# Kernel optimization log

Measured on AMD Instinct MI355X. Metric: run time of the kernel, lower is better.

## Reference

```python
import jax, jax.numpy as jnp
import numpy as np

N_PATIENT = 50000
N_GENE = 20000
N_EDGE = 640000
P_DIM, G_DIM, H, OUT = 64, 32, 128, 8


def setup_inputs() -> dict:
    key = jax.random.key(0)
    ks = jax.random.split(key, 20)
    s = 0.02
    return {
        "x_patient": jax.random.normal(ks[0], (N_PATIENT, P_DIM), jnp.float32),
        "x_gene": jax.random.normal(ks[1], (N_GENE, G_DIM), jnp.float32),
        "edge_index": jax.random.randint(ks[2], (2, N_EDGE), 0, N_GENE, jnp.int32),
        # patient MLP
        "W_p1": jax.random.normal(ks[3], (P_DIM, H), jnp.float32) * s,
        "b_p1": jnp.zeros((H,), jnp.float32),
        "W_p2": jax.random.normal(ks[4], (H, H), jnp.float32) * s,
        "b_p2": jnp.zeros((H,), jnp.float32),
        # gene MLP
        "W_g1": jax.random.normal(ks[5], (G_DIM, H), jnp.float32) * s,
        "b_g1": jnp.zeros((H,), jnp.float32),
        "W_g2": jax.random.normal(ks[6], (H, H), jnp.float32) * s,
        "b_g2": jnp.zeros((H,), jnp.float32),
        # SAGEConv 1: lin_l acts on aggregated src, lin_r (root) on dst
        "W1_l": jax.random.normal(ks[7], (H, H), jnp.float32) * s,
        "b1_l": jnp.zeros((H,), jnp.float32),
        "W1_r": jax.random.normal(ks[8], (H, H), jnp.float32) * s,
        # SAGEConv 2
        "W2_l": jax.random.normal(ks[9], (H, H), jnp.float32) * s,
        "b2_l": jnp.zeros((H,), jnp.float32),
        "W2_r": jax.random.normal(ks[10], (H, H), jnp.float32) * s,
        # final fc
        "W_fc": jax.random.normal(ks[11], (H, OUT), jnp.float32) * s,
        "b_fc": jnp.zeros((OUT,), jnp.float32),
    }


def reference(x_patient, x_gene, edge_index,
              W_p1, b_p1, W_p2, b_p2,
              W_g1, b_g1, W_g2, b_g2,
              W1_l, b1_l, W1_r,
              W2_l, b2_l, W2_r,
              W_fc, b_fc):
    # node-type MLPs
    p = jax.nn.relu(x_patient @ W_p1 + b_p1) @ W_p2 + b_p2   # [N_P, H]
    g = jax.nn.relu(x_gene @ W_g1 + b_g1) @ W_g2 + b_g2       # [N_G, H]

    src, dst = edge_index[0], edge_index[1]
    # gene_x is unchanged between layers, so the sum-aggregate is identical
    # for both SAGEConv layers: compute the gather + segment-sum once.
    agg = jax.ops.segment_sum(g[src], dst, num_segments=x_patient.shape[0])  # [N_P, H]

    # SAGEConv(aggr='sum'): out = lin_l(agg) + lin_r(x_dst), bias in lin_l
    p = jax.nn.relu(agg @ W1_l + b1_l + p @ W1_r)
    p = jax.nn.relu(agg @ W2_l + b2_l + p @ W2_r)
    return p @ W_fc + b_fc  # [N_P, OUT]
```

## Files before the change

### kernel.cpp

```cpp
#include <hip/hip_runtime.h>

#define NP 50000
#define NG 20000
#define NE 640000
#define PD 64
#define GD 32
#define HD 128
#define OD 8
#define CAP 96
#define FILLB 125
#define EPB 5120
#define GENE_TILES 313
#define ROW0_NOAGG 20096
#define AGGPAD (ROW0_NOAGG - NG)
#define PATALLB 782

using f32x4 = __attribute__((ext_vector_type(4))) float;
using s16x8 = __attribute__((ext_vector_type(8))) short;

__device__ __forceinline__ unsigned short f2bf(float f) {
    union { float f; unsigned u; } v; v.f = f;
    const unsigned r = v.u + 0x7FFFu + ((v.u >> 16) & 1u);
    return (unsigned short)(r >> 16);
}
__device__ __forceinline__ float bfpair_lo(unsigned v) {
    union { unsigned u; float f; } x; x.u = v << 16; return x.f;
}
__device__ __forceinline__ float bfpair_hi(unsigned v) {
    union { unsigned u; float f; } x; x.u = v & 0xFFFF0000u; return x.f;
}

#define TOT_SWZ 112640

__global__ __launch_bounds__(256) void swz_kernel(
    const float* __restrict__ Wp1, const float* __restrict__ Wp2,
    const float* __restrict__ W1l, const float* __restrict__ W1r,
    const float* __restrict__ W2l, const float* __restrict__ W2r,
    const float* __restrict__ Wfc,
    const float* __restrict__ Wg1, const float* __restrict__ Wg2,
    unsigned short* __restrict__ wswz, unsigned short* __restrict__ aggb)
{
    const int u = blockIdx.x * 256 + threadIdx.x;
    if (u < TOT_SWZ) {
        const float* src; int K, Nr, doff;
        if      (u <   8192) { src = Wp1; K =  64; Nr = HD; doff = 0; }
        else if (u <  24576) { src = Wp2; K = 128; Nr = HD; doff = 8192; }
        else if (u <  40960) { src = W1l; K = 128; Nr = HD; doff = 24576; }
        else if (u <  57344) { src = W1r; K = 128; Nr = HD; doff = 40960; }
        else if (u <  73728) { src = W2l; K = 128; Nr = HD; doff = 57344; }
        else if (u <  90112) { src = W2r; K = 128; Nr = HD; doff = 73728; }
        else if (u <  92160) { src = Wfc; K = 128; Nr = OD; doff = 90112; }
        else if (u <  96256) { src = Wg1; K =  32; Nr = HD; doff = 92160; }
        else                 { src = Wg2; K = 128; Nr = HD; doff = 96256; }
        const int e  = u - doff;
        const int j  = e & 7;
        const int ln = (e >> 3) & 63;
        const int f  = e >> 9;
        const int KC = K >> 5;
        const int c  = f % KC;
        const int n0 = f / KC;
        const int k  = c * 32 + (ln >> 4) * 8 + j;
        const int n  = n0 * 16 + (ln & 15);
        wswz[u] = f2bf((n < Nr) ? src[k * Nr + n] : 0.f);
    } else {
        aggb[(size_t)NG * HD + (u - TOT_SWZ)] = 0;
    }
}

__global__ __launch_bounds__(256) void genefill_kernel(
    const float* __restrict__ xg,
    const unsigned short* __restrict__ wswz,
    const float* __restrict__ bg1, const float* __restrict__ bg2,
    unsigned short* __restrict__ g,
    const int* __restrict__ ei, unsigned short* __restrict__ hist16)
{
    __shared__ __align__(16) char smem[20480];
    const int tid = threadIdx.x;
    if (blockIdx.x >= GENE_TILES) {
        int* cnt = (int*)smem;
#pragma unroll
        for (int k = 0; k < 5; ++k) {
            const int idx = k * 256 + tid;
            if (idx < NG / 16) ((int4*)cnt)[idx] = (int4){0, 0, 0, 0};
        }
        __syncthreads();
        const int fb = blockIdx.x - GENE_TILES;
        const int base = fb * EPB;
#pragma unroll
        for (int it = 0; it < 5; ++it) {
            const int e0 = base + it * 1024 + tid;
            const int d0 = ei[NE + e0];
            const int d1 = ei[NE + e0 + 256];
            const int d2 = ei[NE + e0 + 512];
            const int d3 = ei[NE + e0 + 768];
            atomicAdd(&cnt[d0 >> 2], 1 << ((d0 & 3) * 8));
            atomicAdd(&cnt[d1 >> 2], 1 << ((d1 & 3) * 8));
            atomicAdd(&cnt[d2 >> 2], 1 << ((d2 & 3) * 8));
            atomicAdd(&cnt[d3 >> 2], 1 << ((d3 & 3) * 8));
        }
        __syncthreads();
        unsigned short* Hb = hist16 + fb * NG;
#pragma unroll
        for (int k = 0; k < 20; ++k) {
            const int idx = k * 256 + tid;
            if (idx < NG / 4) {
                const unsigned w = (unsigned)cnt[idx];
                int2 o;
                o.x = (int)((w & 0xFFu) | ((w & 0xFF00u) << 8));
                o.y = (int)(((w >> 16) & 0xFFu) | (((w >> 24) & 0xFFu) << 16));
                ((int2*)Hb)[idx] = o;
            }
        }
        return;
    }
    const unsigned short* wg1 = wswz + 92160;
    const unsigned short* wg2 = wswz + 96256;

    const int lane = tid & 63;
    const int wid  = tid >> 6;
    const int quad = lane >> 4;
    const int l16  = lane & 15;
    const int row0 = blockIdx.x * 64 + wid * 16;
    const int arow = min(row0 + l16, NG - 1);
    unsigned short* X = (unsigned short*)smem + wid * 16 * 136;
    const f32x4 Z = {0.f, 0.f, 0.f, 0.f};

    s16x8 a;
    {
        const float* xr = xg + (size_t)arow * GD + quad * 8;
        const f32x4 u0 = *(const f32x4*)xr;
        const f32x4 u1 = *(const f32x4*)(xr + 4);
#pragma unroll
        for (int j = 0; j < 4; ++j) {
            a[j]     = (short)f2bf(u0[j]);
            a[4 + j] = (short)f2bf(u1[j]);
        }
    }
    f32x4 C[8];
#pragma unroll
    for (int n = 0; n < 8; ++n) {
        const s16x8 b = *(const s16x8*)&wg1[(n * 64 + lane) * 8];
        C[n] = __builtin_amdgcn_mfma_f32_16x16x32_bf16(a, b, Z, 0, 0, 0);
    }
#pragma unroll
    for (int n = 0; n < 8; ++n) {
        const float bias = bg1[n * 16 + l16];
#pragma unroll
        for (int r = 0; r < 4; ++r)
            X[(quad * 4 + r) * 136 + n * 16 + l16] = f2bf(fmaxf(C[n][r] + bias, 0.f));
    }
    __syncthreads();
    s16x8 pa[4];
#pragma unroll
    for (int c = 0; c < 4; ++c) pa[c] = *(const s16x8*)&X[l16 * 136 + c * 32 + quad * 8];
#pragma unroll
    for (int n = 0; n < 8; ++n) {
        C[n] = Z;
#pragma unroll
        for (int c = 0; c < 4; ++c) {
            const s16x8 b = *(const s16x8*)&wg2[((n * 4 + c) * 64 + lane) * 8];
            C[n] = __builtin_amdgcn_mfma_f32_16x16x32_bf16(pa[c], b, C[n], 0, 0, 0);
        }
    }
#pragma unroll
    for (int n = 0; n < 8; ++n) {
        const float bias = bg2[n * 16 + l16];
#pragma unroll
        for (int r = 0; r < 4; ++r) {
            const int row = row0 + quad * 4 + r;
            if (row < NG) g[(size_t)row * HD + n * 16 + l16] = f2bf(C[n][r] + bias);
        }
    }
}

__global__ __launch_bounds__(256) void scan_kernel(
    unsigned short* __restrict__ hist16, int* __restrict__ cursor)
{
    const int d = blockIdx.x * 256 + threadIdx.x;
    if (d >= NG) return;
    int run = 0;
#pragma unroll 5
    for (int b = 0; b < FILLB; ++b) {
        const int t = hist16[b * NG + d];
        hist16[b * NG + d] = (unsigned short)run;
        run += t;
    }
    cursor[d] = run;
}

__global__ __launch_bounds__(256) void place_kernel(
    const int* __restrict__ ei, const unsigned short* __restrict__ hist16,
    unsigned short* __restrict__ pad)
{
    __shared__ __align__(16) int cnt[NG / 2];
    const int tid = threadIdx.x;
    const int* Hb = (const int*)(hist16 + blockIdx.x * NG);
#pragma unroll
    for (int k = 0; k < 10; ++k) {
        const int idx = k * 256 + tid;
        if (idx < NG / 8) ((int4*)cnt)[idx] = ((const int4*)Hb)[idx];
    }
    __syncthreads();
    const int base = blockIdx.x * EPB;
#pragma unroll
    for (int it = 0; it < 5; ++it) {
        const int e0 = base + it * 1024 + tid;
        const int s0 = ei[e0];       const int d0 = ei[NE + e0];
        const int s1 = ei[e0 + 256]; const int d1 = ei[NE + e0 + 256];
        const int s2 = ei[e0 + 512]; const int d2 = ei[NE + e0 + 512];
        const int s3 = ei[e0 + 768]; const int d3 = ei[NE + e0 + 768];
        { const int o = atomicAdd(&cnt[d0 >> 1], 1 << ((d0 & 1) * 16));
          const int p = (o >> ((d0 & 1) * 16)) & 0xFFFF;
          if (p < CAP) pad[d0 * CAP + p] = (unsigned short)s0; }
        { const int o = atomicAdd(&cnt[d1 >> 1], 1 << ((d1 & 1) * 16));
          const int p = (o >> ((d1 & 1) * 16)) & 0xFFFF;
          if (p < CAP) pad[d1 * CAP + p] = (unsigned short)s1; }
        { const int o = atomicAdd(&cnt[d2 >> 1], 1 << ((d2 & 1) * 16));
          const int p = (o >> ((d2 & 1) * 16)) & 0xFFFF;
          if (p < CAP) pad[d2 * CAP + p] = (unsigned short)s2; }
        { const int o = atomicAdd(&cnt[d3 >> 1], 1 << ((d3 & 1) * 16));
          const int p = (o >> ((d3 & 1) * 16)) & 0xFFFF;
          if (p < CAP) pad[d3 * CAP + p] = (unsigned short)s3; }
    }
}

__global__ __launch_bounds__(256) void agg_kernel(
    const int* __restrict__ cursor, const unsigned short* __restrict__ pad,
    const unsigned short* __restrict__ g, unsigned short* __restrict__ aggb)
{
    const int row  = blockIdx.x * 4 + (threadIdx.x >> 6);
    const int lane = threadIdx.x & 63;
    const int grp  = lane >> 4;
    const int sub  = lane & 15;

    float acc[8] = {0.f, 0.f, 0.f, 0.f, 0.f, 0.f, 0.f, 0.f};
    const int cnt = min(cursor[row], CAP);
    const size_t rb = (size_t)row * CAP;
    for (int i = grp * 4; i < cnt; i += 16) {
        const ushort4 q = *(const ushort4*)&pad[rb + i];
        int r0 = q.x, r1 = q.y, r2 = q.z, r3 = q.w;
        const bool v1 = (i + 1) < cnt, v2 = (i + 2) < cnt, v3 = (i + 3) < cnt;
        r1 = v1 ? r1 : r0;  r2 = v2 ? r2 : r0;  r3 = v3 ? r3 : r0;
        const float s1 = v1 ? 1.f : 0.f, s2 = v2 ? 1.f : 0.f, s3 = v3 ? 1.f : 0.f;
        const s16x8 g0 = *(const s16x8*)&g[(size_t)r0 * HD + sub * 8];
        const s16x8 g1 = *(const s16x8*)&g[(size_t)r1 * HD + sub * 8];
        const s16x8 g2 = *(const s16x8*)&g[(size_t)r2 * HD + sub * 8];
        const s16x8 g3 = *(const s16x8*)&g[(size_t)r3 * HD + sub * 8];
        const unsigned* d0 = (const unsigned*)&g0;
        const unsigned* d1 = (const unsigned*)&g1;
        const unsigned* d2 = (const unsigned*)&g2;
        const unsigned* d3 = (const unsigned*)&g3;
#pragma unroll
        for (int k = 0; k < 4; ++k) {
            acc[2 * k]     += bfpair_lo(d0[k]);
            acc[2 * k + 1] += bfpair_hi(d0[k]);
            acc[2 * k]     = fmaf(bfpair_lo(d1[k]), s1, acc[2 * k]);
            acc[2 * k + 1] = fmaf(bfpair_hi(d1[k]), s1, acc[2 * k + 1]);
            acc[2 * k]     = fmaf(bfpair_lo(d2[k]), s2, acc[2 * k]);
            acc[2 * k + 1] = fmaf(bfpair_hi(d2[k]), s2, acc[2 * k + 1]);
            acc[2 * k]     = fmaf(bfpair_lo(d3[k]), s3, acc[2 * k]);
            acc[2 * k + 1] = fmaf(bfpair_hi(d3[k]), s3, acc[2 * k + 1]);
        }
    }
#pragma unroll
    for (int k = 0; k < 8; ++k) {
        acc[k] += __shfl_xor(acc[k], 16);
        acc[k] += __shfl_xor(acc[k], 32);
    }
    if (lane < 16) {
        unsigned o[4];
#pragma unroll
        for (int k = 0; k < 4; ++k)
            o[k] = (unsigned)f2bf(acc[2 * k]) | ((unsigned)f2bf(acc[2 * k + 1]) << 16);
        *(int4*)&aggb[(size_t)row * HD + lane * 8] = *(int4*)o;
    }
}

__global__ __launch_bounds__(256) void patall_kernel(
    const float* __restrict__ xp, const unsigned short* __restrict__ aggb,
    const unsigned short* __restrict__ wswz,
    const float* __restrict__ bp1, const float* __restrict__ bp2,
    const float* __restrict__ b1l, const float* __restrict__ b2l,
    const float* __restrict__ bfc,
    float* __restrict__ out)
{
    const unsigned short* wp1 = wswz + 0;
    const unsigned short* wp2 = wswz + 8192;
    const unsigned short* w1l = wswz + 24576;
    const unsigned short* w1r = wswz + 40960;
    const unsigned short* w2l = wswz + 57344;
    const unsigned short* w2r = wswz + 73728;
    const unsigned short* wfc = wswz + 90112;

    __shared__ __align__(16) unsigned short XA[64 * 136];

    const int tid  = threadIdx.x;
    const int lane = tid & 63;
    const int wid  = tid >> 6;
    const int quad = lane >> 4;
    const int l16  = lane & 15;
    const int brow = blockIdx.x * 64;
    const bool hasAgg = (brow < NG);
    const int nA = wid * 2, nB = wid * 2 + 1;
    const f32x4 Z = {0.f, 0.f, 0.f, 0.f};

#pragma unroll
    for (int s = 0; s < 4; ++s) {
        const int slot = s * 256 + tid;
        const int r  = slot >> 4;
        const int cv = slot & 15;
        const f32x4 u = *(const f32x4*)&xp[(size_t)min(brow + r, NP - 1) * PD + cv * 4];
        unsigned short o[4];
#pragma unroll
        for (int j = 0; j < 4; ++j) o[j] = f2bf(u[j]);
        *(ushort4*)&XA[r * 136 + cv * 4] = *(ushort4*)o;
    }
    __syncthreads();

    f32x4 acc[4][2];

#pragma unroll
    for (int rt = 0; rt < 4; ++rt) { acc[rt][0] = Z; acc[rt][1] = Z; }
#pragma unroll
    for (int c = 0; c < 2; ++c) {
        const s16x8 b0 = *(const s16x8*)&wp1[((nA * 2 + c) * 64 + lane) * 8];
        const s16x8 b1 = *(const s16x8*)&wp1[((nB * 2 + c) * 64 + lane) * 8];
#pragma unroll
        for (int rt = 0; rt < 4; ++rt) {
            const s16x8 a = *(const s16x8*)&XA[(rt * 16 + l16) * 136 + c * 32 + quad * 8];
            acc[rt][0] = __builtin_amdgcn_mfma_f32_16x16x32_bf16(a, b0, acc[rt][0], 0, 0, 0);
            acc[rt][1] = __builtin_amdgcn_mfma_f32_16x16x32_bf16(a, b1, acc[rt][1], 0, 0, 0);
        }
    }
    __syncthreads();
#pragma unroll
    for (int t = 0; t < 2; ++t) {
        const int n = wid * 2 + t;
        const float bias = bp1[n * 16 + l16];
#pragma unroll
        for (int rt = 0; rt < 4; ++rt)
#pragma unroll
            for (int r = 0; r < 4; ++r)
                XA[(rt * 16 + quad * 4 + r) * 136 + n * 16 + l16] =
                    f2bf(fmaxf(acc[rt][t][r] + bias, 0.f));
    }
    __syncthreads();

#pragma unroll
    for (int rt = 0; rt < 4; ++rt) { acc[rt][0] = Z; acc[rt][1] = Z; }
#pragma unroll
    for (int c = 0; c < 4; ++c) {
        const s16x8 b0 = *(const s16x8*)&wp2[((nA * 4 + c) * 64 + lane) * 8];
        const s16x8 b1 = *(const s16x8*)&wp2[((nB * 4 + c) * 64 + lane) * 8];
#pragma unroll
        for (int rt = 0; rt < 4; ++rt) {
            const s16x8 a = *(const s16x8*)&XA[(rt * 16 + l16) * 136 + c * 32 + quad * 8];
            acc[rt][0] = __builtin_amdgcn_mfma_f32_16x16x32_bf16(a, b0, acc[rt][0], 0, 0, 0);
            acc[rt][1] = __builtin_amdgcn_mfma_f32_16x16x32_bf16(a, b1, acc[rt][1], 0, 0, 0);
        }
    }
    __syncthreads();
#pragma unroll
    for (int t = 0; t < 2; ++t) {
        const int n = wid * 2 + t;
        const float bias = bp2[n * 16 + l16];
#pragma unroll
        for (int rt = 0; rt < 4; ++rt)
#pragma unroll
            for (int r = 0; r < 4; ++r)
                XA[(rt * 16 + quad * 4 + r) * 136 + n * 16 + l16] =
                    f2bf(acc[rt][t][r] + bias);
    }
    __syncthreads();

    if (hasAgg) {
#pragma unroll
        for (int rt = 0; rt < 4; ++rt) { acc[rt][0] = Z; acc[rt][1] = Z; }
#pragma unroll
        for (int c = 0; c < 4; ++c) {
            const s16x8 br0 = *(const s16x8*)&w1r[((nA * 4 + c) * 64 + lane) * 8];
            const s16x8 br1 = *(const s16x8*)&w1r[((nB * 4 + c) * 64 + lane) * 8];
            const s16x8 bl0 = *(const s16x8*)&w1l[((nA * 4 + c) * 64 + lane) * 8];
            const s16x8 bl1 = *(const s16x8*)&w1l[((nB * 4 + c) * 64 + lane) * 8];
#pragma unroll
            for (int rt = 0; rt < 4; ++rt) {
                const s16x8 ap = *(const s16x8*)&XA[(rt * 16 + l16) * 136 + c * 32 + quad * 8];
                const s16x8 ag = *(const s16x8*)&aggb[(size_t)(brow + rt * 16 + l16) * HD + c * 32 + quad * 8];
                acc[rt][0] = __builtin_amdgcn_mfma_f32_16x16x32_bf16(ap, br0, acc[rt][0], 0, 0, 0);
                acc[rt][0] = __builtin_amdgcn_mfma_f32_16x16x32_bf16(ag, bl0, acc[rt][0], 0, 0, 0);
                acc[rt][1] = __builtin_amdgcn_mfma_f32_16x16x32_bf16(ap, br1, acc[rt][1], 0, 0, 0);
                acc[rt][1] = __builtin_amdgcn_mfma_f32_16x16x32_bf16(ag, bl1, acc[rt][1], 0, 0, 0);
            }
        }
        __syncthreads();
#pragma unroll
        for (int t = 0; t < 2; ++t) {
            const int n = wid * 2 + t;
            const float bias = b1l[n * 16 + l16];
#pragma unroll
            for (int rt = 0; rt < 4; ++rt)
#pragma unroll
                for (int r = 0; r < 4; ++r)
                    XA[(rt * 16 + quad * 4 + r) * 136 + n * 16 + l16] =
                        f2bf(fmaxf(acc[rt][t][r] + bias, 0.f));
        }
        __syncthreads();

#pragma unroll
        for (int rt = 0; rt < 4; ++rt) { acc[rt][0] = Z; acc[rt][1] = Z; }
#pragma unroll
        for (int c = 0; c < 4; ++c) {
            const s16x8 br0 = *(const s16x8*)&w2r[((nA * 4 + c) * 64 + lane) * 8];
            const s16x8 br1 = *(const s16x8*)&w2r[((nB * 4 + c) * 64 + lane) * 8];
            const s16x8 bl0 = *(const s16x8*)&w2l[((nA * 4 + c) * 64 + lane) * 8];
            const s16x8 bl1 = *(const s16x8*)&w2l[((nB * 4 + c) * 64 + lane) * 8];
#pragma unroll
            for (int rt = 0; rt < 4; ++rt) {
                const s16x8 ap = *(const s16x8*)&XA[(rt * 16 + l16) * 136 + c * 32 + quad * 8];
                const s16x8 ag = *(const s16x8*)&aggb[(size_t)(brow + rt * 16 + l16) * HD + c * 32 + quad * 8];
                acc[rt][0] = __builtin_amdgcn_mfma_f32_16x16x32_bf16(ap, br0, acc[rt][0], 0, 0, 0);
                acc[rt][0] = __builtin_amdgcn_mfma_f32_16x16x32_bf16(ag, bl0, acc[rt][0], 0, 0, 0);
                acc[rt][1] = __builtin_amdgcn_mfma_f32_16x16x32_bf16(ap, br1, acc[rt][1], 0, 0, 0);
                acc[rt][1] = __builtin_amdgcn_mfma_f32_16x16x32_bf16(ag, bl1, acc[rt][1], 0, 0, 0);
            }
        }
        __syncthreads();
#pragma unroll
        for (int t = 0; t < 2; ++t) {
            const int n = wid * 2 + t;
            const float bias = b2l[n * 16 + l16];
#pragma unroll
            for (int rt = 0; rt < 4; ++rt)
#pragma unroll
                for (int r = 0; r < 4; ++r)
                    XA[(rt * 16 + quad * 4 + r) * 136 + n * 16 + l16] =
                        f2bf(fmaxf(acc[rt][t][r] + bias, 0.f));
        }
        __syncthreads();
    } else {
#pragma unroll
        for (int rt = 0; rt < 4; ++rt) { acc[rt][0] = Z; acc[rt][1] = Z; }
#pragma unroll
        for (int c = 0; c < 4; ++c) {
            const s16x8 b0 = *(const s16x8*)&w1r[((nA * 4 + c) * 64 + lane) * 8];
            const s16x8 b1 = *(const s16x8*)&w1r[((nB * 4 + c) * 64 + lane) * 8];
#pragma unroll
            for (int rt = 0; rt < 4; ++rt) {
                const s16x8 a = *(const s16x8*)&XA[(rt * 16 + l16) * 136 + c * 32 + quad * 8];
                acc[rt][0] = __builtin_amdgcn_mfma_f32_16x16x32_bf16(a, b0, acc[rt][0], 0, 0, 0);
                acc[rt][1] = __builtin_amdgcn_mfma_f32_16x16x32_bf16(a, b1, acc[rt][1], 0, 0, 0);
            }
        }
        __syncthreads();
#pragma unroll
        for (int t = 0; t < 2; ++t) {
            const int n = wid * 2 + t;
            const float bias = b1l[n * 16 + l16];
#pragma unroll
            for (int rt = 0; rt < 4; ++rt)
#pragma unroll
                for (int r = 0; r < 4; ++r)
                    XA[(rt * 16 + quad * 4 + r) * 136 + n * 16 + l16] =
                        f2bf(fmaxf(acc[rt][t][r] + bias, 0.f));
        }
        __syncthreads();

#pragma unroll
        for (int rt = 0; rt < 4; ++rt) { acc[rt][0] = Z; acc[rt][1] = Z; }
#pragma unroll
        for (int c = 0; c < 4; ++c) {
            const s16x8 b0 = *(const s16x8*)&w2r[((nA * 4 + c) * 64 + lane) * 8];
            const s16x8 b1 = *(const s16x8*)&w2r[((nB * 4 + c) * 64 + lane) * 8];
#pragma unroll
            for (int rt = 0; rt < 4; ++rt) {
                const s16x8 a = *(const s16x8*)&XA[(rt * 16 + l16) * 136 + c * 32 + quad * 8];
                acc[rt][0] = __builtin_amdgcn_mfma_f32_16x16x32_bf16(a, b0, acc[rt][0], 0, 0, 0);
                acc[rt][1] = __builtin_amdgcn_mfma_f32_16x16x32_bf16(a, b1, acc[rt][1], 0, 0, 0);
            }
        }
        __syncthreads();
#pragma unroll
        for (int t = 0; t < 2; ++t) {
            const int n = wid * 2 + t;
            const float bias = b2l[n * 16 + l16];
#pragma unroll
            for (int rt = 0; rt < 4; ++rt)
#pragma unroll
                for (int r = 0; r < 4; ++r)
                    XA[(rt * 16 + quad * 4 + r) * 136 + n * 16 + l16] =
                        f2bf(fmaxf(acc[rt][t][r] + bias, 0.f));
        }
        __syncthreads();
    }

    {
        f32x4 co = Z;
#pragma unroll
        for (int c = 0; c < 4; ++c) {
            const s16x8 b = *(const s16x8*)&wfc[(c * 64 + lane) * 8];
            const s16x8 a = *(const s16x8*)&XA[(wid * 16 + l16) * 136 + c * 32 + quad * 8];
            co = __builtin_amdgcn_mfma_f32_16x16x32_bf16(a, b, co, 0, 0, 0);
        }
        if (l16 < OD) {
            const float bias = bfc[l16];
#pragma unroll
            for (int r = 0; r < 4; ++r) {
                const int row = brow + wid * 16 + quad * 4 + r;
                if (row < NP) out[(size_t)row * OD + l16] = co[r] + bias;
            }
        }
    }
}

extern "C" void kernel_launch(void* const* d_in, const int* in_sizes, int n_in,
                              void* d_out, int out_size, void* d_ws, size_t ws_size,
                              hipStream_t stream)
{
    const float* xp  = (const float*)d_in[0];
    const float* xg  = (const float*)d_in[1];
    const int*   ei  = (const int*)d_in[2];
    const float* Wp1 = (const float*)d_in[3];
    const float* bp1 = (const float*)d_in[4];
    const float* Wp2 = (const float*)d_in[5];
    const float* bp2 = (const float*)d_in[6];
    const float* Wg1 = (const float*)d_in[7];
    const float* bg1 = (const float*)d_in[8];
    const float* Wg2 = (const float*)d_in[9];
    const float* bg2 = (const float*)d_in[10];
    const float* W1l = (const float*)d_in[11];
    const float* b1l = (const float*)d_in[12];
    const float* W1r = (const float*)d_in[13];
    const float* W2l = (const float*)d_in[14];
    const float* b2l = (const float*)d_in[15];
    const float* W2r = (const float*)d_in[16];
    const float* Wfc = (const float*)d_in[17];
    const float* bfc = (const float*)d_in[18];
    float* out = (float*)d_out;

    char* ws = (char*)d_ws;
    unsigned short* g_b    = (unsigned short*)(ws + 0);
    unsigned short* wswz   = (unsigned short*)(ws + 5120000);
    int*            cursor = (int*)(ws + 5345280);
    unsigned short* hist16 = (unsigned short*)(ws + 5425280);
    unsigned short* pad    = (unsigned short*)(ws + 10425280);
    unsigned short* agg_b  = (unsigned short*)(ws + 14265280);

    swz_kernel<<<(TOT_SWZ + AGGPAD * HD) / 256, 256, 0, stream>>>(
        Wp1, Wp2, W1l, W1r, W2l, W2r, Wfc, Wg1, Wg2, wswz, agg_b);

    genefill_kernel<<<GENE_TILES + FILLB, 256, 0, stream>>>(
        xg, wswz, bg1, bg2, g_b, ei, hist16);

    scan_kernel<<<(NG + 255) / 256, 256, 0, stream>>>(hist16, cursor);

    place_kernel<<<FILLB, 256, 0, stream>>>(ei, hist16, pad);

    agg_kernel<<<NG / 4, 256, 0, stream>>>(cursor, pad, g_b, agg_b);

    patall_kernel<<<PATALLB, 256, 0, stream>>>(
        xp, agg_b, wswz, bp1, bp2, b1l, b2l, bfc, out);
}
```

Before: 165.1 us.

## Fuse gene-to-patient aggregation into patient MLP kernel via LDS tile

Removes the separate aggregation kernel and its global bf16 agg buffer. Each patient block that owns rows with incoming edges gathers and sums gene features itself into a shared-memory tile, which the two SAGE layers then read from LDS. Block IDs are interleaved so gather-heavy blocks alternate with MLP-only blocks, spreading load across CUs. This saves a launch and a global write/read of the aggregate, at the cost of more LDS per block, lower occupancy, and a serial 16-row gather loop per wave inside the fused kernel.

New measurement: 185.6 us. 12.4% more time.

```diff
diff --git a/kernel.cpp b/kernel.cpp
--- a/kernel.cpp
+++ b/kernel.cpp
@@ -11,8 +11,9 @@
 #define FILLB 125
 #define EPB 5120
 #define GENE_TILES 313
-#define ROW0_NOAGG 20096
-#define AGGPAD (ROW0_NOAGG - NG)
+#define AGG_BLKS 313
+#define NOAGG0 20032
+#define NOAGG_BLKS 469
 #define PATALLB 782
 
 using f32x4 = __attribute__((ext_vector_type(4))) float;
@@ -38,7 +39,7 @@
     const float* __restrict__ W2l, const float* __restrict__ W2r,
     const float* __restrict__ Wfc,
     const float* __restrict__ Wg1, const float* __restrict__ Wg2,
-    unsigned short* __restrict__ wswz, unsigned short* __restrict__ aggb)
+    unsigned short* __restrict__ wswz)
 {
     const int u = blockIdx.x * 256 + threadIdx.x;
     if (u < TOT_SWZ) {
@@ -62,8 +63,6 @@
         const int k  = c * 32 + (ln >> 4) * 8 + j;
         const int n  = n0 * 16 + (ln & 15);
         wswz[u] = f2bf((n < Nr) ? src[k * Nr + n] : 0.f);
-    } else {
-        aggb[(size_t)NG * HD + (u - TOT_SWZ)] = 0;
     }
 }
 
@@ -224,60 +223,10 @@
     }
 }
 
-__global__ __launch_bounds__(256) void agg_kernel(
+__global__ __launch_bounds__(256) void patall_kernel(
+    const float* __restrict__ xp,
+    const unsigned short* __restrict__ g,
     const int* __restrict__ cursor, const unsigned short* __restrict__ pad,
-    const unsigned short* __restrict__ g, unsigned short* __restrict__ aggb)
-{
-    const int row  = blockIdx.x * 4 + (threadIdx.x >> 6);
-    const int lane = threadIdx.x & 63;
-    const int grp  = lane >> 4;
-    const int sub  = lane & 15;
-
-    float acc[8] = {0.f, 0.f, 0.f, 0.f, 0.f, 0.f, 0.f, 0.f};
-    const int cnt = min(cursor[row], CAP);
-    const size_t rb = (size_t)row * CAP;
-    for (int i = grp * 4; i < cnt; i += 16) {
-        const ushort4 q = *(const ushort4*)&pad[rb + i];
-        int r0 = q.x, r1 = q.y, r2 = q.z, r3 = q.w;
-        const bool v1 = (i + 1) < cnt, v2 = (i + 2) < cnt, v3 = (i + 3) < cnt;
-        r1 = v1 ? r1 : r0;  r2 = v2 ? r2 : r0;  r3 = v3 ? r3 : r0;
-        const float s1 = v1 ? 1.f : 0.f, s2 = v2 ? 1.f : 0.f, s3 = v3 ? 1.f : 0.f;
-        const s16x8 g0 = *(const s16x8*)&g[(size_t)r0 * HD + sub * 8];
-        const s16x8 g1 = *(const s16x8*)&g[(size_t)r1 * HD + sub * 8];
-        const s16x8 g2 = *(const s16x8*)&g[(size_t)r2 * HD + sub * 8];
-        const s16x8 g3 = *(const s16x8*)&g[(size_t)r3 * HD + sub * 8];
-        const unsigned* d0 = (const unsigned*)&g0;
-        const unsigned* d1 = (const unsigned*)&g1;
-        const unsigned* d2 = (const unsigned*)&g2;
-        const unsigned* d3 = (const unsigned*)&g3;
-#pragma unroll
-        for (int k = 0; k < 4; ++k) {
-            acc[2 * k]     += bfpair_lo(d0[k]);
-            acc[2 * k + 1] += bfpair_hi(d0[k]);
-            acc[2 * k]     = fmaf(bfpair_lo(d1[k]), s1, acc[2 * k]);
-            acc[2 * k + 1] = fmaf(bfpair_hi(d1[k]), s1, acc[2 * k + 1]);
-            acc[2 * k]     = fmaf(bfpair_lo(d2[k]), s2, acc[2 * k]);
-            acc[2 * k + 1] = fmaf(bfpair_hi(d2[k]), s2, acc[2 * k + 1]);
-            acc[2 * k]     = fmaf(bfpair_lo(d3[k]), s3, acc[2 * k]);
-            acc[2 * k + 1] = fmaf(bfpair_hi(d3[k]), s3, acc[2 * k + 1]);
-        }
-    }
-#pragma unroll
-    for (int k = 0; k < 8; ++k) {
-        acc[k] += __shfl_xor(acc[k], 16);
-        acc[k] += __shfl_xor(acc[k], 32);
-    }
-    if (lane < 16) {
-        unsigned o[4];
-#pragma unroll
-        for (int k = 0; k < 4; ++k)
-            o[k] = (unsigned)f2bf(acc[2 * k]) | ((unsigned)f2bf(acc[2 * k + 1]) << 16);
-        *(int4*)&aggb[(size_t)row * HD + lane * 8] = *(int4*)o;
-    }
-}
-
-__global__ __launch_bounds__(256) void patall_kernel(
-    const float* __restrict__ xp, const unsigned short* __restrict__ aggb,
     const unsigned short* __restrict__ wswz,
     const float* __restrict__ bp1, const float* __restrict__ bp2,
     const float* __restrict__ b1l, const float* __restrict__ b2l,
@@ -293,14 +242,22 @@
     const unsigned short* wfc = wswz + 90112;
 
     __shared__ __align__(16) unsigned short XA[64 * 136];
+    __shared__ __align__(16) unsigned short AG[64 * 136];
 
     const int tid  = threadIdx.x;
     const int lane = tid & 63;
     const int wid  = tid >> 6;
     const int quad = lane >> 4;
     const int l16  = lane & 15;
-    const int brow = blockIdx.x * 64;
-    const bool hasAgg = (brow < NG);
+    const int bid  = blockIdx.x;
+
+    bool hasAgg; int brow;
+    if ((bid & 1) && (bid >> 1) < AGG_BLKS) {
+        hasAgg = true;  brow = (bid >> 1) * 64;
+    } else {
+        const int nid = (bid & 1) ? (391 + ((bid - 627) >> 1)) : (bid >> 1);
+        hasAgg = false; brow = NOAGG0 + nid * 64;
+    }
     const int nA = wid * 2, nB = wid * 2 + 1;
     const f32x4 Z = {0.f, 0.f, 0.f, 0.f};
 
@@ -315,6 +272,56 @@
         for (int j = 0; j < 4; ++j) o[j] = f2bf(u[j]);
         *(ushort4*)&XA[r * 136 + cv * 4] = *(ushort4*)o;
     }
+
+    if (hasAgg) {
+        const int grp = lane >> 4;
+        const int sub = lane & 15;
+        for (int rr = 0; rr < 16; ++rr) {
+            const int lrow = wid * 16 + rr;
+            const int row  = brow + lrow;
+            float acc[8] = {0.f, 0.f, 0.f, 0.f, 0.f, 0.f, 0.f, 0.f};
+            const int cnt = (row < NG) ? min(cursor[row], CAP) : 0;
+            const size_t rb = (size_t)row * CAP;
+            for (int i = grp * 4; i < cnt; i += 16) {
+                const ushort4 q = *(const ushort4*)&pad[rb + i];
+                int r0 = q.x, r1 = q.y, r2 = q.z, r3 = q.w;
+                const bool v1 = (i + 1) < cnt, v2 = (i + 2) < cnt, v3 = (i + 3) < cnt;
+                r1 = v1 ? r1 : r0;  r2 = v2 ? r2 : r0;  r3 = v3 ? r3 : r0;
+                const float s1 = v1 ? 1.f : 0.f, s2 = v2 ? 1.f : 0.f, s3 = v3 ? 1.f : 0.f;
+                const s16x8 g0 = *(const s16x8*)&g[(size_t)r0 * HD + sub * 8];
+                const s16x8 g1 = *(const s16x8*)&g[(size_t)r1 * HD + sub * 8];
+                const s16x8 g2 = *(const s16x8*)&g[(size_t)r2 * HD + sub * 8];
+                const s16x8 g3 = *(const s16x8*)&g[(size_t)r3 * HD + sub * 8];
+                const unsigned* d0 = (const unsigned*)&g0;
+                const unsigned* d1 = (const unsigned*)&g1;
+                const unsigned* d2 = (const unsigned*)&g2;
+                const unsigned* d3 = (const unsigned*)&g3;
+#pragma unroll
+                for (int k = 0; k < 4; ++k) {
+                    acc[2 * k]     += bfpair_lo(d0[k]);
+                    acc[2 * k + 1] += bfpair_hi(d0[k]);
+                    acc[2 * k]     = fmaf(bfpair_lo(d1[k]), s1, acc[2 * k]);
+                    acc[2 * k + 1] = fmaf(bfpair_hi(d1[k]), s1, acc[2 * k + 1]);
+                    acc[2 * k]     = fmaf(bfpair_lo(d2[k]), s2, acc[2 * k]);
+                    acc[2 * k + 1] = fmaf(bfpair_hi(d2[k]), s2, acc[2 * k + 1]);
+                    acc[2 * k]     = fmaf(bfpair_lo(d3[k]), s3, acc[2 * k]);
+                    acc[2 * k + 1] = fmaf(bfpair_hi(d3[k]), s3, acc[2 * k + 1]);
+                }
+            }
+#pragma unroll
+            for (int k = 0; k < 8; ++k) {
+                acc[k] += __shfl_xor(acc[k], 16);
+                acc[k] += __shfl_xor(acc[k], 32);
+            }
+            if (lane < 16) {
+                unsigned o[4];
+#pragma unroll
+                for (int k = 0; k < 4; ++k)
+                    o[k] = (unsigned)f2bf(acc[2 * k]) | ((unsigned)f2bf(acc[2 * k + 1]) << 16);
+                *(int4*)&AG[lrow * 136 + lane * 8] = *(int4*)o;
+            }
+        }
+    }
     __syncthreads();
 
     f32x4 acc[4][2];
@@ -385,7 +392,7 @@
 #pragma unroll
             for (int rt = 0; rt < 4; ++rt) {
                 const s16x8 ap = *(const s16x8*)&XA[(rt * 16 + l16) * 136 + c * 32 + quad * 8];
-                const s16x8 ag = *(const s16x8*)&aggb[(size_t)(brow + rt * 16 + l16) * HD + c * 32 + quad * 8];
+                const s16x8 ag = *(const s16x8*)&AG[(rt * 16 + l16) * 136 + c * 32 + quad * 8];
                 acc[rt][0] = __builtin_amdgcn_mfma_f32_16x16x32_bf16(ap, br0, acc[rt][0], 0, 0, 0);
                 acc[rt][0] = __builtin_amdgcn_mfma_f32_16x16x32_bf16(ag, bl0, acc[rt][0], 0, 0, 0);
                 acc[rt][1] = __builtin_amdgcn_mfma_f32_16x16x32_bf16(ap, br1, acc[rt][1], 0, 0, 0);
@@ -417,7 +424,7 @@
 #pragma unroll
             for (int rt = 0; rt < 4; ++rt) {
                 const s16x8 ap = *(const s16x8*)&XA[(rt * 16 + l16) * 136 + c * 32 + quad * 8];
-                const s16x8 ag = *(const s16x8*)&aggb[(size_t)(brow + rt * 16 + l16) * HD + c * 32 + quad * 8];
+                const s16x8 ag = *(const s16x8*)&AG[(rt * 16 + l16) * 136 + c * 32 + quad * 8];
                 acc[rt][0] = __builtin_amdgcn_mfma_f32_16x16x32_bf16(ap, br0, acc[rt][0], 0, 0, 0);
                 acc[rt][0] = __builtin_amdgcn_mfma_f32_16x16x32_bf16(ag, bl0, acc[rt][0], 0, 0, 0);
                 acc[rt][1] = __builtin_amdgcn_mfma_f32_16x16x32_bf16(ap, br1, acc[rt][1], 0, 0, 0);
@@ -543,10 +550,9 @@
     int*            cursor = (int*)(ws + 5345280);
     unsigned short* hist16 = (unsigned short*)(ws + 5425280);
     unsigned short* pad    = (unsigned short*)(ws + 10425280);
-    unsigned short* agg_b  = (unsigned short*)(ws + 14265280);
-
-    swz_kernel<<<(TOT_SWZ + AGGPAD * HD) / 256, 256, 0, stream>>>(
-        Wp1, Wp2, W1l, W1r, W2l, W2r, Wfc, Wg1, Wg2, wswz, agg_b);
+
+    swz_kernel<<<(TOT_SWZ + 255) / 256, 256, 0, stream>>>(
+        Wp1, Wp2, W1l, W1r, W2l, W2r, Wfc, Wg1, Wg2, wswz);
 
     genefill_kernel<<<GENE_TILES + FILLB, 256, 0, stream>>>(
         xg, wswz, bg1, bg2, g_b, ei, hist16);
@@ -555,8 +561,6 @@
 
     place_kernel<<<FILLB, 256, 0, stream>>>(ei, hist16, pad);
 
-    agg_kernel<<<NG / 4, 256, 0, stream>>>(cursor, pad, g_b, agg_b);
-
     patall_kernel<<<PATALLB, 256, 0, stream>>>(
-        xp, agg_b, wswz, bp1, bp2, b1l, b2l, bfc, out);
-}
+        xp, g_b, cursor, pad, wswz, bp1, bp2, b1l, b2l, bfc, out);
+}
```
